# Kernel tuning notes

Measured on AMD Instinct MI355X. Metric: run time of the kernel, lower is better.

## Reference

```python
import jax, jax.numpy as jnp
import numpy as np

EMBED_DIM = 1024
NUM_HEADS = 16
HEAD_DIM = EMBED_DIM // NUM_HEADS
GLOBAL_HEADS = 1
LOCAL_K = 128
SCALE = HEAD_DIM ** -0.5


def setup_inputs() -> dict:
    key = jax.random.key(0)
    ks = jax.random.split(key, 9)
    B, n = 4, 2048
    s = 1.0 / np.sqrt(EMBED_DIM)  # torch Linear default uniform(-1/sqrt(in), 1/sqrt(in))
    def lin(k):
        kw, kb = jax.random.split(k)
        W = jax.random.uniform(kw, (EMBED_DIM, EMBED_DIM), jnp.float32, -s, s)
        b = jax.random.uniform(kb, (EMBED_DIM,), jnp.float32, -s, s)
        return W, b
    wq, bq = lin(ks[0])
    wk, bk = lin(ks[1])
    wv, bv = lin(ks[2])
    wo, bo = lin(ks[3])
    x = jax.random.normal(ks[4], (B, n, EMBED_DIM), jnp.float32)
    return {"x": x, "wq": wq, "bq": bq, "wk": wk, "bk": bk,
            "wv": wv, "bv": bv, "wo": wo, "bo": bo}


def _attend(x, wq, bq, wk, bk, wv, bv, wo, bo):
    B, n, E = x.shape
    H, D = NUM_HEADS, HEAD_DIM
    def proj(W, b):
        t = x @ W.T + b                       # [B, n, E]
        return t.reshape(B, n, H, D).transpose(0, 2, 1, 3)  # [B, H, n, D]
    q, k, v = proj(wq, bq), proj(wk, bk), proj(wv, bv)
    scores = jnp.einsum('bhqd,bhkd->bhqk', q, k) * SCALE  # [B, H, n, n]
    idx = jnp.arange(n)
    band = jnp.abs(idx[:, None] - idx[None, :]) <= LOCAL_K  # [n, n] True = allowed
    is_global = jnp.arange(H) < GLOBAL_HEADS
    mask = band[None, :, :] | is_global[:, None, None]      # [H, n, n]
    scores = jnp.where(mask[None], scores, -jnp.inf)
    attn = jax.nn.softmax(scores, axis=-1)   # dropout is identity (p=0 / eval)
    out = jnp.einsum('bhqk,bhkd->bhqd', attn, v)
    out = out.transpose(0, 2, 1, 3).reshape(B, n, E)
    return out @ wo.T + bo


def reference(x, wq, bq, wk, bk, wv, bv, wo, bo):
    return _attend(x, wq, bq, wk, bk, wv, bv, wo, bo)
```

## Files before the change

kernel.cpp:

```cpp
#include <hip/hip_runtime.h>

typedef __attribute__((ext_vector_type(4))) float f32x4;
typedef __attribute__((ext_vector_type(8))) short s16x8;

#define GLDS(gsrc, ldst) \
  __builtin_amdgcn_global_load_lds((const __attribute__((address_space(1))) void*)(gsrc), \
                                   (__attribute__((address_space(3))) void*)(ldst), 16, 0, 0)

__device__ __forceinline__ ushort f2bf(float f) {
  union { float f; unsigned u; } x; x.f = f;
  unsigned r = (x.u + 0x7FFFu + ((x.u >> 16) & 1u)) >> 16;
  return (ushort)r;
}

__global__ __launch_bounds__(256) void castall(
    const float* __restrict__ x, const float* __restrict__ wq, const float* __restrict__ wk,
    const float* __restrict__ wv, const float* __restrict__ wo,
    ushort* __restrict__ xb, ushort* __restrict__ wqkvb, ushort* __restrict__ wob) {
  int bid = blockIdx.x;
  const float* in; ushort* op;
  if (bid < 8192)       { in = x;  op = xb; }
  else if (bid < 9216)  { in = wq; op = wqkvb;           bid -= 8192; }
  else if (bid < 10240) { in = wk; op = wqkvb + 1048576; bid -= 9216; }
  else if (bid < 11264) { in = wv; op = wqkvb + 2097152; bid -= 10240; }
  else                  { in = wo; op = wob;             bid -= 11264; }
  int i = (bid * 256 + threadIdx.x) * 4;
  float4 v = *(const float4*)(in + i);
  ushort4 r;
  r.x = f2bf(v.x); r.y = f2bf(v.y); r.z = f2bf(v.z); r.w = f2bf(v.w);
  *(ushort4*)(op + i) = r;
}

template<int OUTBF16>
__global__ __launch_bounds__(512, 2) void gemm256(
    const ushort* __restrict__ A, const ushort* __restrict__ Bt,
    const float* __restrict__ bias0, const float* __restrict__ bias1,
    const float* __restrict__ bias2,
    void* __restrict__ Cout, int M, int N, int K, int nxn)
{
  __shared__ __align__(16) ushort lds[73728];
  const int tid = threadIdx.x;
  const int w = tid >> 6, lane = tid & 63;
  const int lrow = lane & 15, lg = lane >> 4;
  const int wm = w >> 2, wn = w & 3;
  const int cpx = gridDim.x >> 3;
  const int wgid = ((int)blockIdx.x & 7) * cpx + ((int)blockIdx.x >> 3);
  const int mblk = (wgid / nxn) * 128;
  const int nblk = (wgid % nxn) * 256;
  const int NT = K >> 6;

  const int srow = tid >> 3;
  const int scol = 8 * ((tid & 7) ^ (srow & 7));
  const ushort* Abase = A + (size_t)(mblk + srow) * K + scol;
  const ushort* Bbase = Bt + (size_t)(nblk + srow) * K + scol;
  const size_t rstep = (size_t)64 * K;
  const int dA = w * 512;
  const int dB = 8192 + w * 512;

#define STAGE_A(p, bf) { \
    GLDS((p),         &lds[(bf) + dA]); \
    GLDS((p) + rstep, &lds[(bf) + dA + 4096]); }
#define STAGE_B(p, bf) { \
    GLDS((p),             &lds[(bf) + dB]); \
    GLDS((p) + rstep,     &lds[(bf) + dB + 4096]); \
    GLDS((p) + 2 * rstep, &lds[(bf) + dB + 8192]); \
    GLDS((p) + 3 * rstep, &lds[(bf) + dB + 12288]); }

  const int laneA0 = (wm * 64 + lrow) * 64 + ((lg ^ (lrow & 7)) << 3);
  const int laneA1 = (wm * 64 + lrow) * 64 + (((4 + lg) ^ (lrow & 7)) << 3);
  const int laneB0 = 8192 + (wn * 64 + lrow) * 64 + ((lg ^ (lrow & 7)) << 3);
  const int laneB1 = 8192 + (wn * 64 + lrow) * 64 + (((4 + lg) ^ (lrow & 7)) << 3);

  const f32x4 zero = {0.f, 0.f, 0.f, 0.f};
  f32x4 acc[4][4];
#pragma unroll
  for (int m = 0; m < 4; m++)
#pragma unroll
    for (int n = 0; n < 4; n++) acc[m][n] = zero;

  STAGE_A(Abase, 0); STAGE_B(Bbase, 0);
  if (NT > 1) { STAGE_A(Abase + 64, 24576); STAGE_B(Bbase + 64, 24576); }

  const ushort* aP = Abase + 128;
  const ushort* bP = Bbase + 128;
  int bb = 0, bbS = 49152;

  for (int t = 0; t < NT; ++t) {
    if (t < NT - 1) { asm volatile("s_waitcnt vmcnt(6)" ::: "memory"); }
    else            { asm volatile("s_waitcnt vmcnt(0)" ::: "memory"); }
    __builtin_amdgcn_s_barrier();
    const int pA0 = bb + laneA0, pA1 = bb + laneA1;
    const int pB0 = bb + laneB0, pB1 = bb + laneB1;
    const bool pf = (t + 2 < NT);

    if (pf) STAGE_A(aP, bbS);
    {
      s16x8 af[4], bf_[4];
#pragma unroll
      for (int m = 0; m < 4; m++) af[m] = *(const s16x8*)&lds[pA0 + m * 1024];
#pragma unroll
      for (int n = 0; n < 4; n++) bf_[n] = *(const s16x8*)&lds[pB0 + n * 1024];
      __builtin_amdgcn_s_setprio(1);
#pragma unroll
      for (int m = 0; m < 4; m++)
#pragma unroll
        for (int n = 0; n < 4; n++)
          acc[m][n] = __builtin_amdgcn_mfma_f32_16x16x32_bf16(af[m], bf_[n], acc[m][n], 0, 0, 0);
      __builtin_amdgcn_s_setprio(0);
    }
    if (pf) STAGE_B(bP, bbS);
    {
      s16x8 af[4], bf_[4];
#pragma unroll
      for (int m = 0; m < 4; m++) af[m] = *(const s16x8*)&lds[pA1 + m * 1024];
#pragma unroll
      for (int n = 0; n < 4; n++) bf_[n] = *(const s16x8*)&lds[pB1 + n * 1024];
      __builtin_amdgcn_s_setprio(1);
#pragma unroll
      for (int m = 0; m < 4; m++)
#pragma unroll
        for (int n = 0; n < 4; n++)
          acc[m][n] = __builtin_amdgcn_mfma_f32_16x16x32_bf16(af[m], bf_[n], acc[m][n], 0, 0, 0);
      __builtin_amdgcn_s_setprio(0);
    }
    if (pf) { aP += 64; bP += 64; }
    bb  = (bb  == 49152) ? 0 : bb + 24576;
    bbS = (bbS == 49152) ? 0 : bbS + 24576;
  }
#undef STAGE_A
#undef STAGE_B

  float bias_n[4];
#pragma unroll
  for (int n = 0; n < 4; n++) {
    const int col = nblk + wn * 64 + n * 16 + lrow;
    if (bias1) bias_n[n] = (col < 1024) ? bias0[col]
                          : (col < 2048 ? bias1[col - 1024] : bias2[col - 2048]);
    else bias_n[n] = bias0[col];
  }

  __syncthreads();

  if (OUTBF16) {
    ushort* Ct = lds;
#pragma unroll
    for (int m = 0; m < 4; m++)
#pragma unroll
      for (int n = 0; n < 4; n++)
#pragma unroll
        for (int i = 0; i < 4; i++)
          Ct[(wm * 64 + m * 16 + 4 * lg + i) * 256 + wn * 64 + n * 16 + lrow] =
              f2bf(acc[m][n][i] + bias_n[n]);
    __syncthreads();
    ushort* Cg = (ushort*)Cout;
#pragma unroll
    for (int r = 0; r < 8; r++) {
      const int row = r * 16 + (tid >> 5);
      const int col = (tid & 31) * 8;
      *(s16x8*)&Cg[(size_t)(mblk + row) * N + nblk + col] = *(const s16x8*)&lds[r * 4096 + tid * 8];
    }
  } else {
    float* Cf = (float*)lds;
#pragma unroll
    for (int m = 0; m < 4; m++)
#pragma unroll
      for (int n = 0; n < 4; n++)
#pragma unroll
        for (int i = 0; i < 4; i++)
          Cf[(wm * 64 + m * 16 + 4 * lg + i) * 256 + wn * 64 + n * 16 + lrow] =
              acc[m][n][i] + bias_n[n];
    __syncthreads();
    float* Cg = (float*)Cout;
#pragma unroll
    for (int r = 0; r < 16; r++) {
      const int row = r * 8 + (tid >> 6);
      const int col = (tid & 63) * 4;
      *(float4*)&Cg[(size_t)(mblk + row) * N + nblk + col] = *(const float4*)&Cf[r * 2048 + tid * 4];
    }
  }
}

__global__ __launch_bounds__(256) void attn_kernel(const ushort* __restrict__ qkv,
                                                   ushort* __restrict__ outp,
                                                   float* __restrict__ oPart,
                                                   float* __restrict__ mPart,
                                                   float* __restrict__ lPart)
{
  __shared__ __align__(16) ushort Ks[2][64 * 64];
  __shared__ __align__(16) ushort Vt[2][64 * 64];
  __shared__ __align__(16) ushort Ps[4][16 * 40];

  const int tid = threadIdx.x;
  const int w = tid >> 6, lane = tid & 63;
  const int lrow = lane & 15, lg = lane >> 4;

  const int bid = (blockIdx.x & 7) * 368 + (blockIdx.x >> 3);
  int h, b, bx, kv_lo, kv_hi, chunk = 0;
  bool isGlobal;
  if (bid < 1024) {
    isGlobal = true; h = 0;
    chunk = bid >> 7;
    int qb = bid & 127;
    b = qb >> 5; bx = qb & 31;
    kv_lo = chunk * 256; kv_hi = kv_lo + 256;
  } else {
    isGlobal = false;
    int t = bid - 1024;
    h = 1 + (t >> 7);
    int qb = t & 127;
    b = qb >> 5; bx = qb & 31;
    kv_lo = bx * 64 - 128; if (kv_lo < 0) kv_lo = 0;
    kv_hi = bx * 64 + 192; if (kv_hi > 2048) kv_hi = 2048;
  }
  const int q0b = bx * 64;
  const int q0 = q0b + w * 16;
  const ushort* Qp = qkv + (size_t)b * 2048 * 3072 + h * 64;
  const ushort* Kp = Qp + 1024;
  const ushort* Vp = Qp + 2048;

  s16x8 qf0 = *(const s16x8*)(Qp + (size_t)(q0 + lrow) * 3072 + 8 * lg);
  s16x8 qf1 = *(const s16x8*)(Qp + (size_t)(q0 + lrow) * 3072 + 32 + 8 * lg);

  const f32x4 zero = {0.f, 0.f, 0.f, 0.f};
  f32x4 o[4];
  o[0] = zero; o[1] = zero; o[2] = zero; o[3] = zero;
  float mrun = -3e38f, lsum = 0.f;
  const int q_abs = q0 + lrow;
  const float SCL = 0.18033688011112042f;

  const int sp = tid >> 3;
  const int sg = tid & 7;
  const int kr0 = tid >> 3;
  const int kc = tid & 7;
  const int vx = (lrow & 7) ^ (lrow >> 3);

  const ushort* vr0 = Vp + (size_t)(kv_lo + 2 * sp) * 3072 + 8 * sg;
  s16x8 vlo = *(const s16x8*)vr0;
  s16x8 vhi = *(const s16x8*)(vr0 + 3072);
  GLDS(Kp + (size_t)(kv_lo + kr0) * 3072 + 8 * (kc ^ (kr0 & 7)), &Ks[0][w * 512]);
  GLDS(Kp + (size_t)(kv_lo + 32 + kr0) * 3072 + 8 * (kc ^ (kr0 & 7)), &Ks[0][2048 + w * 512]);

  int buf = 0;
  for (int kv = kv_lo; kv < kv_hi; kv += 64) {
    const bool needMask = !isGlobal && (kv < q0b - 64 || kv + 64 > q0b + 128);
    const bool hasNext = (kv + 64 < kv_hi);

    s16x8 vlon, vhin;
    if (hasNext) {
      const ushort* vr = Vp + (size_t)(kv + 64 + 2 * sp) * 3072 + 8 * sg;
      vlon = *(const s16x8*)vr;
      vhin = *(const s16x8*)(vr + 3072);
    }

#pragma unroll
    for (int j = 0; j < 8; j++) {
      const int d = 8 * sg + j;
      const int r = 2 * sp;
      uint pk = (uint)(ushort)vlo[j] | ((uint)(ushort)vhi[j] << 16);
      *(uint*)&Vt[buf][d * 64 + ((((r >> 3) ^ j ^ sg) & 7) << 3) + (r & 7)] = pk;
    }
    if (hasNext) asm volatile("s_waitcnt vmcnt(2)" ::: "memory");
    else         asm volatile("s_waitcnt vmcnt(0)" ::: "memory");
    asm volatile("s_waitcnt lgkmcnt(0)" ::: "memory");
    __builtin_amdgcn_s_barrier();
    if (hasNext) {
      GLDS(Kp + (size_t)(kv + 64 + kr0) * 3072 + 8 * (kc ^ (kr0 & 7)), &Ks[buf ^ 1][w * 512]);
      GLDS(Kp + (size_t)(kv + 96 + kr0) * 3072 + 8 * (kc ^ (kr0 & 7)), &Ks[buf ^ 1][2048 + w * 512]);
    }

#pragma unroll
    for (int s = 0; s < 2; s++) {
      const int kb = kv + 32 * s;
      const int rs = 32 * s;
      s16x8 kA0 = *(const s16x8*)&Ks[buf][(rs + lrow) * 64      + ((( lg      ^ (lrow & 7)) & 7) << 3)];
      s16x8 kA1 = *(const s16x8*)&Ks[buf][(rs + lrow) * 64      + ((((4 + lg) ^ (lrow & 7)) & 7) << 3)];
      s16x8 kB0 = *(const s16x8*)&Ks[buf][(rs + 16 + lrow) * 64 + ((( lg      ^ (lrow & 7)) & 7) << 3)];
      s16x8 kB1 = *(const s16x8*)&Ks[buf][(rs + 16 + lrow) * 64 + ((((4 + lg) ^ (lrow & 7)) & 7) << 3)];

      f32x4 sA = __builtin_amdgcn_mfma_f32_16x16x32_bf16(kA0, qf0, zero, 0, 0, 0);
      sA = __builtin_amdgcn_mfma_f32_16x16x32_bf16(kA1, qf1, sA, 0, 0, 0);
      f32x4 sB = __builtin_amdgcn_mfma_f32_16x16x32_bf16(kB0, qf0, zero, 0, 0, 0);
      sB = __builtin_amdgcn_mfma_f32_16x16x32_bf16(kB1, qf1, sB, 0, 0, 0);

      float pA[4], pB[4];
      float rowmax = -3e38f;
      if (needMask) {
#pragma unroll
        for (int i = 0; i < 4; i++) {
          int kaA = kb + 4 * lg + i;
          int dq = q_abs - kaA;
          float va = (dq <= 128 && dq >= -128) ? sA[i] * SCL : -1e30f;
          pA[i] = va; rowmax = fmaxf(rowmax, va);
          int dqb = dq - 16;
          float vb = (dqb <= 128 && dqb >= -128) ? sB[i] * SCL : -1e30f;
          pB[i] = vb; rowmax = fmaxf(rowmax, vb);
        }
      } else {
#pragma unroll
        for (int i = 0; i < 4; i++) {
          pA[i] = sA[i] * SCL; pB[i] = sB[i] * SCL;
          rowmax = fmaxf(rowmax, fmaxf(pA[i], pB[i]));
        }
      }
      rowmax = fmaxf(rowmax, __shfl_xor(rowmax, 16));
      rowmax = fmaxf(rowmax, __shfl_xor(rowmax, 32));

      if (!__all(rowmax <= mrun + 8.f)) {
        float mnew = fmaxf(mrun, rowmax);
        float alpha = exp2f(mrun - mnew);
        mrun = mnew;
        lsum *= alpha;
        float a0 = __shfl(alpha, 4 * lg + 0);
        float a1 = __shfl(alpha, 4 * lg + 1);
        float a2 = __shfl(alpha, 4 * lg + 2);
        float a3 = __shfl(alpha, 4 * lg + 3);
#pragma unroll
        for (int c = 0; c < 4; c++) {
          o[c][0] *= a0; o[c][1] *= a1; o[c][2] *= a2; o[c][3] *= a3;
        }
      }

      float rsum = 0.f;
      if (needMask) {
#pragma unroll
        for (int i = 0; i < 4; i++) {
          pA[i] = (pA[i] > -1e29f) ? exp2f(pA[i] - mrun) : 0.f;
          pB[i] = (pB[i] > -1e29f) ? exp2f(pB[i] - mrun) : 0.f;
          rsum += pA[i] + pB[i];
        }
      } else {
#pragma unroll
        for (int i = 0; i < 4; i++) {
          pA[i] = exp2f(pA[i] - mrun);
          pB[i] = exp2f(pB[i] - mrun);
          rsum += pA[i] + pB[i];
        }
      }
      rsum += __shfl_xor(rsum, 16);
      rsum += __shfl_xor(rsum, 32);
      lsum += rsum;

      {
        ushort* P = &Ps[w][lrow * 40];
        *(uint*)&P[4 * lg]      = (uint)f2bf(pA[0]) | ((uint)f2bf(pA[1]) << 16);
        *(uint*)&P[4 * lg + 2]  = (uint)f2bf(pA[2]) | ((uint)f2bf(pA[3]) << 16);
        *(uint*)&P[16 + 4 * lg] = (uint)f2bf(pB[0]) | ((uint)f2bf(pB[1]) << 16);
        *(uint*)&P[18 + 4 * lg] = (uint)f2bf(pB[2]) | ((uint)f2bf(pB[3]) << 16);
      }
      s16x8 paf = *(const s16x8*)&Ps[w][lrow * 40 + 8 * lg];

#pragma unroll
      for (int c = 0; c < 4; c++) {
        const int d = 16 * c + lrow;
        s16x8 vf = *(const s16x8*)&Vt[buf][d * 64 + ((((4 * s + lg) ^ vx ^ (2 * c)) & 7) << 3)];
        o[c] = __builtin_amdgcn_mfma_f32_16x16x32_bf16(paf, vf, o[c], 0, 0, 0);
      }
    }

    vlo = vlon; vhi = vhin;
    buf ^= 1;
  }

  if (isGlobal) {
    const size_t rbase = (size_t)(chunk * 4 + b) * 2048 + q0;
    if (lg == 0) {
      mPart[rbase + lrow] = mrun;
      lPart[rbase + lrow] = lsum;
    }
#pragma unroll
    for (int c = 0; c < 4; c++)
#pragma unroll
      for (int i = 0; i < 4; i++)
        oPart[(rbase + 4 * lg + i) * 64 + 16 * c + lrow] = o[c][i];
  } else {
    float li0 = 1.f / __shfl(lsum, 4 * lg + 0);
    float li1 = 1.f / __shfl(lsum, 4 * lg + 1);
    float li2 = 1.f / __shfl(lsum, 4 * lg + 2);
    float li3 = 1.f / __shfl(lsum, 4 * lg + 3);
    size_t orow = (size_t)(b * 2048 + q0 + 4 * lg);
#pragma unroll
    for (int c = 0; c < 4; c++) {
      outp[(orow + 0) * 1024 + h * 64 + 16 * c + lrow] = f2bf(o[c][0] * li0);
      outp[(orow + 1) * 1024 + h * 64 + 16 * c + lrow] = f2bf(o[c][1] * li1);
      outp[(orow + 2) * 1024 + h * 64 + 16 * c + lrow] = f2bf(o[c][2] * li2);
      outp[(orow + 3) * 1024 + h * 64 + 16 * c + lrow] = f2bf(o[c][3] * li3);
    }
  }
}

__global__ __launch_bounds__(256) void combine_kernel(const float* __restrict__ oPart,
                                                      const float* __restrict__ mPart,
                                                      const float* __restrict__ lPart,
                                                      ushort* __restrict__ attno) {
  const int tid = threadIdx.x;
  const int row = blockIdx.x * 64 + (tid >> 2);
  const int d0 = (tid & 3) * 16;
  float m[8], l[8], M = -3e38f;
#pragma unroll
  for (int p = 0; p < 8; p++) {
    m[p] = mPart[p * 8192 + row];
    l[p] = lPart[p * 8192 + row];
    M = fmaxf(M, m[p]);
  }
  float L = 0.f, wgt[8];
#pragma unroll
  for (int p = 0; p < 8; p++) { wgt[p] = exp2f(m[p] - M); L += wgt[p] * l[p]; }
  float inv = 1.f / L;
  float acc[16];
#pragma unroll
  for (int j = 0; j < 16; j++) acc[j] = 0.f;
#pragma unroll
  for (int p = 0; p < 8; p++) {
    const float* op = oPart + ((size_t)p * 8192 + row) * 64 + d0;
    float wv = wgt[p];
#pragma unroll
    for (int j = 0; j < 16; j += 4) {
      float4 v = *(const float4*)(op + j);
      acc[j]     += wv * v.x; acc[j + 1] += wv * v.y;
      acc[j + 2] += wv * v.z; acc[j + 3] += wv * v.w;
    }
  }
  ushort* dst = attno + (size_t)row * 1024 + d0;
#pragma unroll
  for (int j = 0; j < 16; j++) dst[j] = f2bf(acc[j] * inv);
}

extern "C" void kernel_launch(void* const* d_in, const int* in_sizes, int n_in,
                              void* d_out, int out_size, void* d_ws, size_t ws_size,
                              hipStream_t stream) {
  const float* x  = (const float*)d_in[0];
  const float* wq = (const float*)d_in[1];
  const float* bq = (const float*)d_in[2];
  const float* wk = (const float*)d_in[3];
  const float* bk = (const float*)d_in[4];
  const float* wv = (const float*)d_in[5];
  const float* bv = (const float*)d_in[6];
  const float* wo = (const float*)d_in[7];
  const float* bo = (const float*)d_in[8];

  char* ws = (char*)d_ws;
  ushort* xb    = (ushort*)(ws);
  ushort* wqkvb = (ushort*)(ws + 16777216);
  ushort* wob   = (ushort*)(ws + 23068672);
  ushort* qkvb  = (ushort*)(ws + 25165824);
  ushort* attno = (ushort*)(ws + 75497472);
  float* oPart = (float*)(ws);
  float* mPart = (float*)(ws + 16777216);
  float* lPart = (float*)(ws + 16777216 + 262144);

  castall<<<12288, 256, 0, stream>>>(x, wq, wk, wv, wo, xb, wqkvb, wob);

  gemm256<1><<<768, 512, 0, stream>>>(xb, wqkvb, bq, bk, bv,
                                      (void*)qkvb, 8192, 3072, 1024, 12);

  attn_kernel<<<2944, 256, 0, stream>>>(qkvb, attno, oPart, mPart, lPart);
  combine_kernel<<<128, 256, 0, stream>>>(oPart, mPart, lPart, attno);

  gemm256<0><<<256, 512, 0, stream>>>(attno, wob, bo, nullptr, nullptr,
                                      (void*)d_out, 8192, 1024, 1024, 4);
}
```

Baseline: 172.4 us.

## Switch attention to 32x32x16 MFMA with 2 waves per block and register P

Rewrites the attention kernel so each of two waves handles 32 query rows using 32x32x16 bf16 MFMAs instead of four waves on 16 rows with 16x16x32. The softmax probabilities are packed to bf16 and exchanged between lane halves with shuffles, so they no longer round-trip through a shared-memory P buffer. K and V staging is reworked for 128 threads, with four rows of V per thread and four K load-to-LDS issues per tile. The aim is fewer MFMA issues and LDS operations per tile and a simpler row-max reduction, at the cost of more accumulator registers and halved threads per block, which may affect occupancy and latency hiding.

Measured after the change: 166.8 us. -3.3%, faster.

```diff
diff --git a/kernel.cpp b/kernel.cpp
--- a/kernel.cpp
+++ b/kernel.cpp
@@ -1,6 +1,7 @@
 #include <hip/hip_runtime.h>
 
 typedef __attribute__((ext_vector_type(4))) float f32x4;
+typedef __attribute__((ext_vector_type(16))) float f32x16;
 typedef __attribute__((ext_vector_type(8))) short s16x8;
 
 #define GLDS(gsrc, ldst) \
@@ -11,6 +12,19 @@
   union { float f; unsigned u; } x; x.f = f;
   unsigned r = (x.u + 0x7FFFu + ((x.u >> 16) & 1u)) >> 16;
   return (ushort)r;
+}
+
+__device__ __forceinline__ uint pkbf(float a, float b) {
+  union { float f; uint u; } x, y; x.f = a; y.f = b;
+  uint lo = (x.u + 0x7FFFu + ((x.u >> 16) & 1u)) >> 16;
+  uint hiw = (y.u + 0x7FFFu + ((y.u >> 16) & 1u)) & 0xFFFF0000u;
+  return lo | hiw;
+}
+
+__device__ __forceinline__ s16x8 mk_frag(uint x0, uint x1, uint x2, uint x3) {
+  union { uint u[4]; s16x8 v; } t;
+  t.u[0] = x0; t.u[1] = x1; t.u[2] = x2; t.u[3] = x3;
+  return t.v;
 }
 
 __global__ __launch_bounds__(256) void castall(
@@ -180,19 +194,18 @@
   }
 }
 
-__global__ __launch_bounds__(256) void attn_kernel(const ushort* __restrict__ qkv,
-                                                   ushort* __restrict__ outp,
-                                                   float* __restrict__ oPart,
-                                                   float* __restrict__ mPart,
-                                                   float* __restrict__ lPart)
+__global__ __launch_bounds__(128, 2) void attn_kernel(const ushort* __restrict__ qkv,
+                                                      ushort* __restrict__ outp,
+                                                      float* __restrict__ oPart,
+                                                      float* __restrict__ mPart,
+                                                      float* __restrict__ lPart)
 {
-  __shared__ __align__(16) ushort Ks[2][64 * 64];
-  __shared__ __align__(16) ushort Vt[2][64 * 64];
-  __shared__ __align__(16) ushort Ps[4][16 * 40];
+  __shared__ __align__(16) ushort Ks[2][4096];
+  __shared__ __align__(16) ushort Vt[2][4096];
 
   const int tid = threadIdx.x;
   const int w = tid >> 6, lane = tid & 63;
-  const int lrow = lane & 15, lg = lane >> 4;
+  const int lq = lane & 31, hi = lane >> 5;
 
   const int bid = (blockIdx.x & 7) * 368 + (blockIdx.x >> 3);
   int h, b, bx, kv_lo, kv_hi, chunk = 0;
@@ -213,177 +226,176 @@
     kv_hi = bx * 64 + 192; if (kv_hi > 2048) kv_hi = 2048;
   }
   const int q0b = bx * 64;
-  const int q0 = q0b + w * 16;
+  const int q0w = q0b + w * 32;
+  const int q_abs = q0w + lq;
   const ushort* Qp = qkv + (size_t)b * 2048 * 3072 + h * 64;
   const ushort* Kp = Qp + 1024;
   const ushort* Vp = Qp + 2048;
 
-  s16x8 qf0 = *(const s16x8*)(Qp + (size_t)(q0 + lrow) * 3072 + 8 * lg);
-  s16x8 qf1 = *(const s16x8*)(Qp + (size_t)(q0 + lrow) * 3072 + 32 + 8 * lg);
-
-  const f32x4 zero = {0.f, 0.f, 0.f, 0.f};
-  f32x4 o[4];
-  o[0] = zero; o[1] = zero; o[2] = zero; o[3] = zero;
+  s16x8 qf[4];
+#pragma unroll
+  for (int c = 0; c < 4; c++)
+    qf[c] = *(const s16x8*)(Qp + (size_t)q_abs * 3072 + 16 * c + 8 * hi);
+
+  f32x16 o0, o1;
+#pragma unroll
+  for (int r = 0; r < 16; r++) { o0[r] = 0.f; o1[r] = 0.f; }
   float mrun = -3e38f, lsum = 0.f;
-  const int q_abs = q0 + lrow;
   const float SCL = 0.18033688011112042f;
 
-  const int sp = tid >> 3;
-  const int sg = tid & 7;
-  const int kr0 = tid >> 3;
-  const int kc = tid & 7;
-  const int vx = (lrow & 7) ^ (lrow >> 3);
-
-  const ushort* vr0 = Vp + (size_t)(kv_lo + 2 * sp) * 3072 + 8 * sg;
-  s16x8 vlo = *(const s16x8*)vr0;
-  s16x8 vhi = *(const s16x8*)(vr0 + 3072);
-  GLDS(Kp + (size_t)(kv_lo + kr0) * 3072 + 8 * (kc ^ (kr0 & 7)), &Ks[0][w * 512]);
-  GLDS(Kp + (size_t)(kv_lo + 32 + kr0) * 3072 + 8 * (kc ^ (kr0 & 7)), &Ks[0][2048 + w * 512]);
+  const int kr = tid >> 3, kc = tid & 7;
+  const int vsp = tid >> 3, vsg = tid & 7;
+  const int kswz = 8 * (kc ^ (kr & 7));
+
+  const ushort* vr0 = Vp + (size_t)(kv_lo + 4 * vsp) * 3072 + 8 * vsg;
+  s16x8 v0 = *(const s16x8*)vr0;
+  s16x8 v1 = *(const s16x8*)(vr0 + 3072);
+  s16x8 v2 = *(const s16x8*)(vr0 + 6144);
+  s16x8 v3 = *(const s16x8*)(vr0 + 9216);
+#pragma unroll
+  for (int i = 0; i < 4; i++)
+    GLDS(Kp + (size_t)(kv_lo + 16 * i + kr) * 3072 + kswz, &Ks[0][i * 1024 + w * 512]);
 
   int buf = 0;
   for (int kv = kv_lo; kv < kv_hi; kv += 64) {
     const bool needMask = !isGlobal && (kv < q0b - 64 || kv + 64 > q0b + 128);
     const bool hasNext = (kv + 64 < kv_hi);
 
-    s16x8 vlon, vhin;
+    s16x8 vn0, vn1, vn2, vn3;
     if (hasNext) {
-      const ushort* vr = Vp + (size_t)(kv + 64 + 2 * sp) * 3072 + 8 * sg;
-      vlon = *(const s16x8*)vr;
-      vhin = *(const s16x8*)(vr + 3072);
+      const ushort* vr = Vp + (size_t)(kv + 64 + 4 * vsp) * 3072 + 8 * vsg;
+      vn0 = *(const s16x8*)vr;
+      vn1 = *(const s16x8*)(vr + 3072);
+      vn2 = *(const s16x8*)(vr + 6144);
+      vn3 = *(const s16x8*)(vr + 9216);
     }
 
 #pragma unroll
     for (int j = 0; j < 8; j++) {
-      const int d = 8 * sg + j;
-      const int r = 2 * sp;
-      uint pk = (uint)(ushort)vlo[j] | ((uint)(ushort)vhi[j] << 16);
-      *(uint*)&Vt[buf][d * 64 + ((((r >> 3) ^ j ^ sg) & 7) << 3) + (r & 7)] = pk;
-    }
-    if (hasNext) asm volatile("s_waitcnt vmcnt(2)" ::: "memory");
+      const int d = 8 * vsg + j;
+      const int sl = ((vsp >> 1) ^ j ^ vsg) & 7;
+      const int a0 = d * 64 + sl * 8 + ((4 * vsp) & 7);
+      *(uint*)&Vt[buf][a0]     = (uint)(ushort)v0[j] | ((uint)(ushort)v1[j] << 16);
+      *(uint*)&Vt[buf][a0 + 2] = (uint)(ushort)v2[j] | ((uint)(ushort)v3[j] << 16);
+    }
+    if (hasNext) asm volatile("s_waitcnt vmcnt(4)" ::: "memory");
     else         asm volatile("s_waitcnt vmcnt(0)" ::: "memory");
     asm volatile("s_waitcnt lgkmcnt(0)" ::: "memory");
     __builtin_amdgcn_s_barrier();
     if (hasNext) {
-      GLDS(Kp + (size_t)(kv + 64 + kr0) * 3072 + 8 * (kc ^ (kr0 & 7)), &Ks[buf ^ 1][w * 512]);
-      GLDS(Kp + (size_t)(kv + 96 + kr0) * 3072 + 8 * (kc ^ (kr0 & 7)), &Ks[buf ^ 1][2048 + w * 512]);
-    }
-
-#pragma unroll
-    for (int s = 0; s < 2; s++) {
-      const int kb = kv + 32 * s;
-      const int rs = 32 * s;
-      s16x8 kA0 = *(const s16x8*)&Ks[buf][(rs + lrow) * 64      + ((( lg      ^ (lrow & 7)) & 7) << 3)];
-      s16x8 kA1 = *(const s16x8*)&Ks[buf][(rs + lrow) * 64      + ((((4 + lg) ^ (lrow & 7)) & 7) << 3)];
-      s16x8 kB0 = *(const s16x8*)&Ks[buf][(rs + 16 + lrow) * 64 + ((( lg      ^ (lrow & 7)) & 7) << 3)];
-      s16x8 kB1 = *(const s16x8*)&Ks[buf][(rs + 16 + lrow) * 64 + ((((4 + lg) ^ (lrow & 7)) & 7) << 3)];
-
-      f32x4 sA = __builtin_amdgcn_mfma_f32_16x16x32_bf16(kA0, qf0, zero, 0, 0, 0);
-      sA = __builtin_amdgcn_mfma_f32_16x16x32_bf16(kA1, qf1, sA, 0, 0, 0);
-      f32x4 sB = __builtin_amdgcn_mfma_f32_16x16x32_bf16(kB0, qf0, zero, 0, 0, 0);
-      sB = __builtin_amdgcn_mfma_f32_16x16x32_bf16(kB1, qf1, sB, 0, 0, 0);
-
-      float pA[4], pB[4];
-      float rowmax = -3e38f;
-      if (needMask) {
-#pragma unroll
-        for (int i = 0; i < 4; i++) {
-          int kaA = kb + 4 * lg + i;
-          int dq = q_abs - kaA;
-          float va = (dq <= 128 && dq >= -128) ? sA[i] * SCL : -1e30f;
-          pA[i] = va; rowmax = fmaxf(rowmax, va);
-          int dqb = dq - 16;
-          float vb = (dqb <= 128 && dqb >= -128) ? sB[i] * SCL : -1e30f;
-          pB[i] = vb; rowmax = fmaxf(rowmax, vb);
-        }
-      } else {
-#pragma unroll
-        for (int i = 0; i < 4; i++) {
-          pA[i] = sA[i] * SCL; pB[i] = sB[i] * SCL;
-          rowmax = fmaxf(rowmax, fmaxf(pA[i], pB[i]));
-        }
+#pragma unroll
+      for (int i = 0; i < 4; i++)
+        GLDS(Kp + (size_t)(kv + 64 + 16 * i + kr) * 3072 + kswz, &Ks[buf ^ 1][i * 1024 + w * 512]);
+    }
+
+    f32x16 s0, s1;
+#pragma unroll
+    for (int r = 0; r < 16; r++) { s0[r] = 0.f; s1[r] = 0.f; }
+#pragma unroll
+    for (int c = 0; c < 4; c++) {
+      const int gx = ((2 * c + hi) ^ (lq & 7)) << 3;
+      s16x8 kf0 = *(const s16x8*)&Ks[buf][lq * 64 + gx];
+      s16x8 kf1 = *(const s16x8*)&Ks[buf][(32 + lq) * 64 + gx];
+      s0 = __builtin_amdgcn_mfma_f32_32x32x16_bf16(kf0, qf[c], s0, 0, 0, 0);
+      s1 = __builtin_amdgcn_mfma_f32_32x32x16_bf16(kf1, qf[c], s1, 0, 0, 0);
+    }
+
+    float rm = -3e38f;
+    if (needMask) {
+#pragma unroll
+      for (int r = 0; r < 16; r++) {
+        const int kvr = kv + (r & 3) + 8 * (r >> 2) + 4 * hi;
+        const int dq0 = q_abs - kvr;
+        s0[r] = (dq0 <= 128 && dq0 >= -128) ? s0[r] * SCL : -1e30f;
+        const int dq1 = dq0 - 32;
+        s1[r] = (dq1 <= 128 && dq1 >= -128) ? s1[r] * SCL : -1e30f;
+        rm = fmaxf(rm, fmaxf(s0[r], s1[r]));
       }
-      rowmax = fmaxf(rowmax, __shfl_xor(rowmax, 16));
-      rowmax = fmaxf(rowmax, __shfl_xor(rowmax, 32));
-
-      if (!__all(rowmax <= mrun + 8.f)) {
-        float mnew = fmaxf(mrun, rowmax);
-        float alpha = exp2f(mrun - mnew);
-        mrun = mnew;
-        lsum *= alpha;
-        float a0 = __shfl(alpha, 4 * lg + 0);
-        float a1 = __shfl(alpha, 4 * lg + 1);
-        float a2 = __shfl(alpha, 4 * lg + 2);
-        float a3 = __shfl(alpha, 4 * lg + 3);
-#pragma unroll
-        for (int c = 0; c < 4; c++) {
-          o[c][0] *= a0; o[c][1] *= a1; o[c][2] *= a2; o[c][3] *= a3;
-        }
+    } else {
+#pragma unroll
+      for (int r = 0; r < 16; r++) {
+        s0[r] *= SCL; s1[r] *= SCL;
+        rm = fmaxf(rm, fmaxf(s0[r], s1[r]));
       }
-
-      float rsum = 0.f;
-      if (needMask) {
-#pragma unroll
-        for (int i = 0; i < 4; i++) {
-          pA[i] = (pA[i] > -1e29f) ? exp2f(pA[i] - mrun) : 0.f;
-          pB[i] = (pB[i] > -1e29f) ? exp2f(pB[i] - mrun) : 0.f;
-          rsum += pA[i] + pB[i];
-        }
-      } else {
-#pragma unroll
-        for (int i = 0; i < 4; i++) {
-          pA[i] = exp2f(pA[i] - mrun);
-          pB[i] = exp2f(pB[i] - mrun);
-          rsum += pA[i] + pB[i];
-        }
+    }
+    rm = fmaxf(rm, __shfl_xor(rm, 32));
+
+    if (!__all(rm <= mrun + 8.f)) {
+      float mnew = fmaxf(mrun, rm);
+      float alpha = exp2f(mrun - mnew);
+      mrun = mnew;
+      lsum *= alpha;
+#pragma unroll
+      for (int r = 0; r < 16; r++) {
+        float av = __shfl(alpha, (r & 3) + 8 * (r >> 2) + 4 * hi);
+        o0[r] *= av; o1[r] *= av;
       }
-      rsum += __shfl_xor(rsum, 16);
-      rsum += __shfl_xor(rsum, 32);
-      lsum += rsum;
-
-      {
-        ushort* P = &Ps[w][lrow * 40];
-        *(uint*)&P[4 * lg]      = (uint)f2bf(pA[0]) | ((uint)f2bf(pA[1]) << 16);
-        *(uint*)&P[4 * lg + 2]  = (uint)f2bf(pA[2]) | ((uint)f2bf(pA[3]) << 16);
-        *(uint*)&P[16 + 4 * lg] = (uint)f2bf(pB[0]) | ((uint)f2bf(pB[1]) << 16);
-        *(uint*)&P[18 + 4 * lg] = (uint)f2bf(pB[2]) | ((uint)f2bf(pB[3]) << 16);
+    }
+
+    float rs = 0.f;
+#pragma unroll
+    for (int r = 0; r < 16; r++) {
+      s0[r] = exp2f(s0[r] - mrun); rs += s0[r];
+      s1[r] = exp2f(s1[r] - mrun); rs += s1[r];
+    }
+    rs += __shfl_xor(rs, 32);
+    lsum += rs;
+
+#pragma unroll
+    for (int cc = 0; cc < 4; cc++) {
+      uint x0, x1, x2, x3;
+      if (cc == 0) { x0 = pkbf(s0[0], s0[1]);  x1 = pkbf(s0[2], s0[3]);
+                     x2 = pkbf(s0[4], s0[5]);  x3 = pkbf(s0[6], s0[7]); }
+      else if (cc == 1) { x0 = pkbf(s0[8], s0[9]);   x1 = pkbf(s0[10], s0[11]);
+                          x2 = pkbf(s0[12], s0[13]); x3 = pkbf(s0[14], s0[15]); }
+      else if (cc == 2) { x0 = pkbf(s1[0], s1[1]);  x1 = pkbf(s1[2], s1[3]);
+                          x2 = pkbf(s1[4], s1[5]);  x3 = pkbf(s1[6], s1[7]); }
+      else { x0 = pkbf(s1[8], s1[9]);   x1 = pkbf(s1[10], s1[11]);
+             x2 = pkbf(s1[12], s1[13]); x3 = pkbf(s1[14], s1[15]); }
+      uint t0 = hi ? x0 : x2;
+      uint t1 = hi ? x1 : x3;
+      uint r0 = __shfl_xor(t0, 32);
+      uint r1 = __shfl_xor(t1, 32);
+      uint w0 = hi ? r0 : x0;
+      uint w1 = hi ? r1 : x1;
+      uint w2 = hi ? x2 : r0;
+      uint w3 = hi ? x3 : r1;
+      s16x8 pa = mk_frag(w0, w1, w2, w3);
+#pragma unroll
+      for (int db = 0; db < 2; db++) {
+        const int d = 32 * db + lq;
+        s16x8 vf = *(const s16x8*)&Vt[buf][d * 64 +
+            ((((2 * cc + hi) ^ (d & 7) ^ (d >> 3)) & 7) << 3)];
+        if (db == 0) o0 = __builtin_amdgcn_mfma_f32_32x32x16_bf16(pa, vf, o0, 0, 0, 0);
+        else         o1 = __builtin_amdgcn_mfma_f32_32x32x16_bf16(pa, vf, o1, 0, 0, 0);
       }
-      s16x8 paf = *(const s16x8*)&Ps[w][lrow * 40 + 8 * lg];
-
-#pragma unroll
-      for (int c = 0; c < 4; c++) {
-        const int d = 16 * c + lrow;
-        s16x8 vf = *(const s16x8*)&Vt[buf][d * 64 + ((((4 * s + lg) ^ vx ^ (2 * c)) & 7) << 3)];
-        o[c] = __builtin_amdgcn_mfma_f32_16x16x32_bf16(paf, vf, o[c], 0, 0, 0);
-      }
-    }
-
-    vlo = vlon; vhi = vhin;
+    }
+
+    v0 = vn0; v1 = vn1; v2 = vn2; v3 = vn3;
     buf ^= 1;
   }
 
   if (isGlobal) {
-    const size_t rbase = (size_t)(chunk * 4 + b) * 2048 + q0;
-    if (lg == 0) {
-      mPart[rbase + lrow] = mrun;
-      lPart[rbase + lrow] = lsum;
-    }
-#pragma unroll
-    for (int c = 0; c < 4; c++)
-#pragma unroll
-      for (int i = 0; i < 4; i++)
-        oPart[(rbase + 4 * lg + i) * 64 + 16 * c + lrow] = o[c][i];
+    const size_t rq = (size_t)(chunk * 4 + b) * 2048 + q0w;
+    if (hi == 0) {
+      mPart[rq + lq] = mrun;
+      lPart[rq + lq] = lsum;
+    }
+#pragma unroll
+    for (int r = 0; r < 16; r++) {
+      const int qr = (r & 3) + 8 * (r >> 2) + 4 * hi;
+      oPart[(rq + qr) * 64 + lq]      = o0[r];
+      oPart[(rq + qr) * 64 + 32 + lq] = o1[r];
+    }
   } else {
-    float li0 = 1.f / __shfl(lsum, 4 * lg + 0);
-    float li1 = 1.f / __shfl(lsum, 4 * lg + 1);
-    float li2 = 1.f / __shfl(lsum, 4 * lg + 2);
-    float li3 = 1.f / __shfl(lsum, 4 * lg + 3);
-    size_t orow = (size_t)(b * 2048 + q0 + 4 * lg);
-#pragma unroll
-    for (int c = 0; c < 4; c++) {
-      outp[(orow + 0) * 1024 + h * 64 + 16 * c + lrow] = f2bf(o[c][0] * li0);
-      outp[(orow + 1) * 1024 + h * 64 + 16 * c + lrow] = f2bf(o[c][1] * li1);
-      outp[(orow + 2) * 1024 + h * 64 + 16 * c + lrow] = f2bf(o[c][2] * li2);
-      outp[(orow + 3) * 1024 + h * 64 + 16 * c + lrow] = f2bf(o[c][3] * li3);
+    float linv = 1.f / lsum;
+#pragma unroll
+    for (int r = 0; r < 16; r++) {
+      const int qr = (r & 3) + 8 * (r >> 2) + 4 * hi;
+      float iv = __shfl(linv, qr);
+      size_t orow = (size_t)(b * 2048 + q0w + qr) * 1024 + h * 64;
+      outp[orow + lq]      = f2bf(o0[r] * iv);
+      outp[orow + 32 + lq] = f2bf(o1[r] * iv);
     }
   }
 }
@@ -453,7 +465,7 @@
   gemm256<1><<<768, 512, 0, stream>>>(xb, wqkvb, bq, bk, bv,
                                       (void*)qkvb, 8192, 3072, 1024, 12);
 
-  attn_kernel<<<2944, 256, 0, stream>>>(qkvb, attno, oPart, mPart, lPart);
+  attn_kernel<<<2944, 128, 0, stream>>>(qkvb, attno, oPart, mPart, lPart);
   combine_kernel<<<128, 256, 0, stream>>>(oPart, mPart, lPart, attno);
 
   gemm256<0><<<256, 512, 0, stream>>>(attno, wob, bo, nullptr, nullptr,
```
